# Kernel tuning notes

Measured on AMD Instinct MI355X. Metric: run time of the kernel, lower is better.

## Reference

```python
import jax, jax.numpy as jnp
import numpy as np

H = W = 256
WS = 8          # window size
SHIFT = 4       # shift size
HEADS = 8
DIM = 128
HD = DIM // HEADS
EPS = 1e-5


def _rel_index():
    # Swin-style relative position index, static constant (N=WS*WS)
    coords = np.stack(np.meshgrid(np.arange(WS), np.arange(WS), indexing='ij')).reshape(2, -1)
    rel = coords[:, :, None] - coords[:, None, :]        # (2, N, N)
    rel = rel + (WS - 1)
    return rel[0] * (2 * WS - 1) + rel[1]                # (N, N) in [0, (2WS-1)^2)

_REL_IDX = _rel_index()


def _ln(x, w, b):
    m = jnp.mean(x, axis=-1, keepdims=True)
    v = jnp.var(x, axis=-1, keepdims=True)
    return (x - m) * jax.lax.rsqrt(v + EPS) * w + b


def setup_inputs() -> dict:
    key = jax.random.key(0)
    ks = jax.random.split(key, 8)
    s = 0.02
    return {
        'x': jax.random.normal(ks[0], (2, H * W, DIM), jnp.float32),
        'norm1_w': jnp.ones((DIM,), jnp.float32),
        'norm1_b': jnp.zeros((DIM,), jnp.float32),
        'qkv_w': jax.random.normal(ks[1], (3 * DIM, DIM), jnp.float32) * s,
        'qkv_b': jnp.zeros((3 * DIM,), jnp.float32),
        'rel_bias_table': jax.random.normal(ks[2], ((2 * WS - 1) ** 2, HEADS), jnp.float32) * s,
        'proj_w': jax.random.normal(ks[3], (DIM, DIM), jnp.float32) * s,
        'proj_b': jnp.zeros((DIM,), jnp.float32),
        'norm2_w': jnp.ones((DIM,), jnp.float32),
        'norm2_b': jnp.zeros((DIM,), jnp.float32),
        'fc1_w': jax.random.normal(ks[4], (4 * DIM, DIM), jnp.float32) * s,
        'fc1_b': jnp.zeros((4 * DIM,), jnp.float32),
        'fc2_w': jax.random.normal(ks[5], (DIM, 4 * DIM), jnp.float32) * s,
        'fc2_b': jnp.zeros((DIM,), jnp.float32),
    }


def reference(x, norm1_w, norm1_b, qkv_w, qkv_b, rel_bias_table, proj_w, proj_b,
              norm2_w, norm2_b, fc1_w, fc1_b, fc2_w, fc2_b):
    B, L, C = x.shape
    N = WS * WS
    shortcut = x

    # norm1 -> spatial -> shift (roll only; original applies no attention mask)
    xs = _ln(x, norm1_w, norm1_b).reshape(B, H, W, C)
    xs = jnp.roll(xs, shift=(-SHIFT, -SHIFT), axis=(1, 2))

    # window partition: (B*nH*nW, N, C)
    win = xs.reshape(B, H // WS, WS, W // WS, WS, C)
    win = win.transpose(0, 1, 3, 2, 4, 5).reshape(-1, N, C)

    # window attention
    qkv = (win @ qkv_w.T + qkv_b).reshape(-1, N, 3, HEADS, HD)
    qkv = qkv.transpose(2, 0, 3, 1, 4)                   # (3, nWin, heads, N, hd)
    q, k, v = qkv[0], qkv[1], qkv[2]
    scale = HD ** -0.5
    attn = jnp.einsum('whnd,whmd->whnm', q * scale, k)   # (nWin, heads, N, N)
    bias = rel_bias_table[_REL_IDX]                      # (N, N, heads)
    attn = attn + bias.transpose(2, 0, 1)[None]
    attn = jax.nn.softmax(attn, axis=-1)
    out = jnp.einsum('whnm,whmd->whnd', attn, v)         # (nWin, heads, N, hd)
    out = out.transpose(0, 2, 1, 3).reshape(-1, N, C)
    out = out @ proj_w.T + proj_b

    # window reverse + un-shift
    out = out.reshape(B, H // WS, W // WS, WS, WS, C)
    out = out.transpose(0, 1, 3, 2, 4, 5).reshape(B, H, W, C)
    out = jnp.roll(out, shift=(SHIFT, SHIFT), axis=(1, 2)).reshape(B, L, C)

    x = shortcut + out

    # MLP (fc1 -> exact GELU -> fc2) with residual
    h = _ln(x, norm2_w, norm2_b)
    h = jax.nn.gelu(h @ fc1_w.T + fc1_b, approximate=False)
    h = h @ fc2_w.T + fc2_b
    return x + h
```

## Files before the change

kernel.cpp:

```cpp
#include <hip/hip_runtime.h>
#include <hip/hip_bf16.h>
#include <cmath>

#define LNEPS 1e-5f

typedef __attribute__((ext_vector_type(8))) short short8v;
typedef __attribute__((ext_vector_type(4))) float f32x4;

__device__ __forceinline__ unsigned short f2bf(float f){
  unsigned u = __float_as_uint(f);
  u += 0x7fffu + ((u >> 16) & 1u);
  return (unsigned short)(u >> 16);
}
__device__ __forceinline__ float gelu_f(float x){
  return 0.5f * x * (1.f + erff(x * 0.70710678118654752f));
}
template <int P>
__device__ __forceinline__ void setprio(){
#ifdef __HIP_DEVICE_COMPILE__
  __builtin_amdgcn_s_setprio(P);
#endif
}

__device__ __forceinline__ f32x4 mfma32(short8v a, short8v b, f32x4 c){
#ifdef __HIP_DEVICE_COMPILE__
  return __builtin_amdgcn_mfma_f32_16x16x32_bf16(a, b, c, 0, 0, 0);
#else
  return c;
#endif
}

__device__ __forceinline__ void stage128(const unsigned short* g, int ldg, short* lds){
#ifdef __HIP_DEVICE_COMPILE__
  const int t = threadIdx.x;
  const int wv = t >> 6;
  #pragma unroll
  for (int it = 0; it < 8; ++it) {
    const int flat = it * 256 + t;
    const int r = flat >> 4, c = flat & 15;
    const unsigned short* src = g + (size_t)r * ldg + ((c ^ (r & 7)) << 3);
    short* dst = lds + (size_t)(it * 256 + wv * 64) * 8;
    __builtin_amdgcn_global_load_lds(
        (const __attribute__((address_space(1))) void*)src,
        (__attribute__((address_space(3))) void*)dst, 16, 0, 0);
  }
#else
  (void)g; (void)ldg; (void)lds;
#endif
}
__device__ __forceinline__ void stage128_512(const unsigned short* g, int ldg, short* lds){
#ifdef __HIP_DEVICE_COMPILE__
  const int t = threadIdx.x;
  const int wv = t >> 6;
  #pragma unroll
  for (int it = 0; it < 4; ++it) {
    const int flat = it * 512 + t;
    const int r = flat >> 4, c = flat & 15;
    const unsigned short* src = g + (size_t)r * ldg + ((c ^ (r & 7)) << 3);
    short* dst = lds + (size_t)(it * 512 + wv * 64) * 8;
    __builtin_amdgcn_global_load_lds(
        (const __attribute__((address_space(1))) void*)src,
        (__attribute__((address_space(3))) void*)dst, 16, 0, 0);
  }
#else
  (void)g; (void)ldg; (void)lds;
#endif
}
__device__ __forceinline__ void stage64(const unsigned short* g, short* lds){
#ifdef __HIP_DEVICE_COMPILE__
  const int t = threadIdx.x;
  const int wv = t >> 6;
  #pragma unroll
  for (int it = 0; it < 4; ++it) {
    const int flat = it * 256 + t;
    const int r = flat >> 4, c = flat & 15;
    const unsigned short* src = g + (size_t)r * 128 + ((c ^ (r & 7)) << 3);
    short* dst = lds + (size_t)(it * 256 + wv * 64) * 8;
    __builtin_amdgcn_global_load_lds(
        (const __attribute__((address_space(1))) void*)src,
        (__attribute__((address_space(3))) void*)dst, 16, 0, 0);
  }
#else
  (void)g; (void)lds;
#endif
}
__device__ __forceinline__ short8v frag_ld(const short* lds, int row, int chunk){
  return *(const short8v*)((const char*)lds + row * 256 + ((chunk ^ (row & 7)) << 4));
}

__global__ __launch_bounds__(256) void k0_cvt(
    const float* __restrict__ qkvw, const float* __restrict__ pw,
    const float* __restrict__ w1, const float* __restrict__ w2,
    unsigned short* __restrict__ dst)
{
  const int i = (blockIdx.x * 256 + threadIdx.x) * 4;
  const float* src; int off;
  if (i < 49152)       { src = qkvw; off = i; }
  else if (i < 65536)  { src = pw;   off = i - 49152; }
  else if (i < 131072) { src = w1;   off = i - 65536; }
  else                 { src = w2;   off = i - 131072; }
  const float4 v = *(const float4*)(src + off);
  ushort4 o = { f2bf(v.x), f2bf(v.y), f2bf(v.z), f2bf(v.w) };
  *(ushort4*)(dst + i) = o;
}

__global__ __launch_bounds__(512, 2) void k23_qkv_attn(
    const float* __restrict__ x,
    const float* __restrict__ gw, const float* __restrict__ gb,
    const unsigned short* __restrict__ Wb,
    const float* __restrict__ bias,
    const float* __restrict__ table,
    unsigned short* __restrict__ attn)
{
  __shared__ __align__(16) short At[128 * 128];
  __shared__ __align__(16) short Bt[128 * 128];
  __shared__ __align__(16) short QKl[128 * 256];
  __shared__ float Tb[1800];
  const int t = threadIdx.x;
  const int row0 = blockIdx.x * 128;
  stage128_512(Wb, 128, At);
  for (int i = t; i < 1800; i += 512) Tb[i] = table[i];
  #pragma unroll
  for (int it = 0; it < 4; ++it) {
    const int flat = it * 512 + t;
    const int r = flat >> 4, c = flat & 15;
    const int row = row0 + r;
    const int wid = row >> 6, n = row & 63;
    const int b = wid >> 10, rem = wid & 1023;
    const int wh = rem >> 5, wwi = rem & 31;
    const int i2 = n >> 3, j2 = n & 7;
    const int sh = (wh * 8 + i2 + 4) & 255;
    const int sw = (wwi * 8 + j2 + 4) & 255;
    const float* src = x + (((size_t)b << 16) + sh * 256 + sw) * 128 + c * 8;
    const float4 a0 = *(const float4*)src;
    const float4 a1 = *(const float4*)(src + 4);
    float s  = a0.x + a0.y + a0.z + a0.w + a1.x + a1.y + a1.z + a1.w;
    float ss = a0.x*a0.x + a0.y*a0.y + a0.z*a0.z + a0.w*a0.w
             + a1.x*a1.x + a1.y*a1.y + a1.z*a1.z + a1.w*a1.w;
    s += __shfl_xor(s, 1); ss += __shfl_xor(ss, 1);
    s += __shfl_xor(s, 2); ss += __shfl_xor(ss, 2);
    s += __shfl_xor(s, 4); ss += __shfl_xor(ss, 4);
    s += __shfl_xor(s, 8); ss += __shfl_xor(ss, 8);
    const float mean = s * 0.0078125f;
    const float rstd = rsqrtf(ss * 0.0078125f - mean * mean + LNEPS);
    const float4 g0 = *(const float4*)(gw + c * 8), g1 = *(const float4*)(gw + c * 8 + 4);
    const float4 c0 = *(const float4*)(gb + c * 8), c1 = *(const float4*)(gb + c * 8 + 4);
    uint4 pk;
    pk.x = (unsigned)f2bf((a0.x - mean) * rstd * g0.x + c0.x)
         | ((unsigned)f2bf((a0.y - mean) * rstd * g0.y + c0.y) << 16);
    pk.y = (unsigned)f2bf((a0.z - mean) * rstd * g0.z + c0.z)
         | ((unsigned)f2bf((a0.w - mean) * rstd * g0.w + c0.w) << 16);
    pk.z = (unsigned)f2bf((a1.x - mean) * rstd * g1.x + c1.x)
         | ((unsigned)f2bf((a1.y - mean) * rstd * g1.y + c1.y) << 16);
    pk.w = (unsigned)f2bf((a1.z - mean) * rstd * g1.z + c1.z)
         | ((unsigned)f2bf((a1.w - mean) * rstd * g1.w + c1.w) << 16);
    *(uint4*)((char*)Bt + r * 256 + ((c ^ (r & 7)) << 4)) = pk;
  }
  __syncthreads();

  const int l = t & 63, w = t >> 6, w0 = w & 1, w1 = w >> 1;
  const int g = l >> 4, rl = l & 15;
  const f32x4 z = {0.f, 0.f, 0.f, 0.f};

  for (int nt = 0; nt < 3; ++nt) {
    f32x4 acc[4][2];
    #pragma unroll
    for (int i = 0; i < 4; ++i) { acc[i][0] = z; acc[i][1] = z; }
    #pragma unroll
    for (int kk = 0; kk < 4; ++kk) {
      short8v a[4], b[2];
      #pragma unroll
      for (int i = 0; i < 4; ++i) a[i] = frag_ld(At, w0 * 64 + i * 16 + rl, kk * 4 + g);
      #pragma unroll
      for (int j = 0; j < 2; ++j) b[j] = frag_ld(Bt, w1 * 32 + j * 16 + rl, kk * 4 + g);
      #pragma unroll
      for (int i = 0; i < 4; ++i)
        #pragma unroll
        for (int j = 0; j < 2; ++j)
          acc[i][j] = mfma32(a[i], b[j], acc[i][j]);
    }
    if (nt < 2) {
      #pragma unroll
      for (int i = 0; i < 4; ++i) {
        const int c = w0 * 64 + i * 16 + 4 * g;
        const float4 bv = *(const float4*)(bias + nt * 128 + c);
        const int chunk = nt * 16 + (c >> 3), inner = (c & 7) * 2;
        #pragma unroll
        for (int j = 0; j < 2; ++j) {
          const int r = w1 * 32 + j * 16 + rl;
          ushort4 o = { f2bf(acc[i][j][0] + bv.x), f2bf(acc[i][j][1] + bv.y),
                        f2bf(acc[i][j][2] + bv.z), f2bf(acc[i][j][3] + bv.w) };
          *(ushort4*)((char*)QKl + r * 512 + ((chunk ^ (r & 7)) << 4) + inner) = o;
        }
      }
      __syncthreads();
      stage128_512(Wb + (size_t)(nt + 1) * 16384, 128, At);
      __syncthreads();
    } else {
      __syncthreads();
      #pragma unroll
      for (int i = 0; i < 4; ++i) {
        const int c = w0 * 64 + i * 16 + 4 * g;
        const int h2 = c >> 4, db = c & 15;
        const float4 bv = *(const float4*)(bias + 256 + c);
        const float ba[4] = {bv.x, bv.y, bv.z, bv.w};
        #pragma unroll
        for (int j = 0; j < 2; ++j) {
          const int r = w1 * 32 + j * 16 + rl;
          const int wl = r >> 6, m = r & 63;
          char* vb = (char*)Bt + (wl * 8 + h2) * 2048;
          #pragma unroll
          for (int e = 0; e < 4; ++e) {
            const int d = db + e;
            *(unsigned short*)(vb + d * 128 + (((m >> 3) ^ (d & 7)) << 4) + (m & 7) * 2)
                = f2bf(acc[i][j][e] + ba[e]);
          }
        }
      }
      __syncthreads();
    }
  }

  const int h = w;
  char* Pw = (char*)At + w * 4096;
  const short8v zz = {0,0,0,0,0,0,0,0};
  for (int wl = 0; wl < 2; ++wl) {
    const int win = blockIdx.x * 2 + wl;
    short8v qf[4], kf[4];
    if (g < 2) {
      #pragma unroll
      for (int rf = 0; rf < 4; ++rf) {
        const int r = wl * 64 + rf * 16 + rl;
        qf[rf] = *(const short8v*)((char*)QKl + r * 512 + (((2 * h + g) ^ (r & 7)) << 4));
      }
      #pragma unroll
      for (int mf = 0; mf < 4; ++mf) {
        const int r = wl * 64 + mf * 16 + rl;
        kf[mf] = *(const short8v*)((char*)QKl + r * 512 + (((16 + 2 * h + g) ^ (r & 7)) << 4));
      }
    } else {
      #pragma unroll
      for (int i = 0; i < 4; ++i) { qf[i] = zz; kf[i] = zz; }
    }
    f32x4 s[4][4];
    #pragma unroll
    for (int mf = 0; mf < 4; ++mf)
      #pragma unroll
      for (int rf = 0; rf < 4; ++rf)
        s[mf][rf] = mfma32(kf[mf], qf[rf], z);
    float sum[4];
    #pragma unroll
    for (int rf = 0; rf < 4; ++rf) {
      const int r = rf * 16 + rl, i1 = r >> 3, j1 = r & 7;
      float mx = -1e30f;
      #pragma unroll
      for (int mf = 0; mf < 4; ++mf)
        #pragma unroll
        for (int e = 0; e < 4; ++e) {
          const int m = mf * 16 + g * 4 + e;
          const int i2 = m >> 3, j2 = m & 7;
          const float v = s[mf][rf][e] * 0.25f + Tb[((i1 - i2 + 7) * 15 + (j1 - j2 + 7)) * 8 + h];
          s[mf][rf][e] = v;
          mx = fmaxf(mx, v);
        }
      mx = fmaxf(mx, __shfl_xor(mx, 16));
      mx = fmaxf(mx, __shfl_xor(mx, 32));
      float sm = 0.f;
      #pragma unroll
      for (int mf = 0; mf < 4; ++mf)
        #pragma unroll
        for (int e = 0; e < 4; ++e) {
          const float ev = __expf(s[mf][rf][e] - mx);
          s[mf][rf][e] = ev;
          sm += ev;
        }
      sm += __shfl_xor(sm, 16);
      sm += __shfl_xor(sm, 32);
      sum[rf] = sm;
    }
    const char* vbase = (char*)Bt + (wl * 8 + h) * 2048;
    f32x4 o[4];
    #pragma unroll
    for (int rf = 0; rf < 4; ++rf) o[rf] = z;
    #pragma unroll
    for (int hm = 0; hm < 2; ++hm) {
      #pragma unroll
      for (int rf = 0; rf < 4; ++rf) {
        const int r = rf * 16 + rl;
        #pragma unroll
        for (int mfl = 0; mfl < 2; ++mfl) {
          const int mf = hm * 2 + mfl;
          uint2 u;
          u.x = (unsigned)f2bf(s[mf][rf][0]) | ((unsigned)f2bf(s[mf][rf][1]) << 16);
          u.y = (unsigned)f2bf(s[mf][rf][2]) | ((unsigned)f2bf(s[mf][rf][3]) << 16);
          *(uint2*)(Pw + r * 64 + (((mfl * 2 + (g >> 1)) ^ ((r >> 1) & 3)) << 4) + (g & 1) * 8) = u;
        }
      }
      const short8v va = *(const short8v*)(vbase + rl * 128 + (((hm * 4 + g) ^ (rl & 7)) << 4));
      #pragma unroll
      for (int rf = 0; rf < 4; ++rf) {
        const int r = rf * 16 + rl;
        const short8v pb = *(const short8v*)(Pw + r * 64 + ((g ^ ((r >> 1) & 3)) << 4));
        o[rf] = mfma32(va, pb, o[rf]);
      }
    }
    #pragma unroll
    for (int rf = 0; rf < 4; ++rf) {
      const float inv = 1.f / sum[rf];
      const int r = rf * 16 + rl;
      ushort4 ov = { f2bf(o[rf][0] * inv), f2bf(o[rf][1] * inv),
                     f2bf(o[rf][2] * inv), f2bf(o[rf][3] * inv) };
      *(ushort4*)(attn + ((size_t)win * 64 + r) * 128 + h * 16 + g * 4) = ov;
    }
  }
}

__global__ __launch_bounds__(256, 2) void k45_proj_mlp(
    const unsigned short* __restrict__ A,
    const unsigned short* __restrict__ pwb,
    const float* __restrict__ pb,
    const float* __restrict__ xin,
    const float* __restrict__ gw, const float* __restrict__ gb,
    const unsigned short* __restrict__ w1b, const float* __restrict__ b1,
    const unsigned short* __restrict__ w2b, const float* __restrict__ b2,
    float* __restrict__ out)
{
  __shared__ __align__(16) short Xt[64 * 128];
  __shared__ __align__(16) short Ht[64 * 128];
  __shared__ __align__(16) short Wt[128 * 128];
  __shared__ float2 Gt[1024];
  __shared__ float2 Red[64 * 8];
  const int t = threadIdx.x;
  const int row0 = blockIdx.x * 64;
  stage128(pwb, 128, Wt);
  stage64(A + (size_t)row0 * 128, Ht);
  #pragma unroll
  for (int i = t; i < 1024; i += 256) {
    const float x0 = (float)i * 0.0078125f - 4.f;
    const float g0 = gelu_f(x0);
    Gt[i] = make_float2(g0, gelu_f(x0 + 0.0078125f) - g0);
  }
  const int l = t & 63, w = t >> 6, w0 = w & 1, w1 = w >> 1;
  const int g = l >> 4, rl = l & 15;
  size_t obase[2];
  float4 xv[4][2];
  #pragma unroll
  for (int j = 0; j < 2; ++j) {
    const int r = row0 + w1 * 32 + j * 16 + rl;
    const int wn = r >> 6, n = r & 63;
    const int b_ = wn >> 10, rem = wn & 1023;
    const int wh = rem >> 5, ww = rem & 31;
    const int si = n >> 3, sj = n & 7;
    const int hd = (wh * 8 + si + 4) & 255;
    const int wd = (ww * 8 + sj + 4) & 255;
    obase[j] = (((size_t)b_ << 16) + hd * 256 + wd) * 128;
    #pragma unroll
    for (int i = 0; i < 4; ++i)
      xv[i][j] = *(const float4*)(xin + obase[j] + w0 * 64 + i * 16 + 4 * g);
  }
  __syncthreads();
  const f32x4 z = {0.f, 0.f, 0.f, 0.f};
  f32x4 x2r[4][2];
  #pragma unroll
  for (int i = 0; i < 4; ++i) { x2r[i][0] = z; x2r[i][1] = z; }
  setprio<1>();
  #pragma unroll
  for (int kk = 0; kk < 4; ++kk) {
    short8v a[4], b[2];
    #pragma unroll
    for (int i = 0; i < 4; ++i) a[i] = frag_ld(Wt, w0 * 64 + i * 16 + rl, kk * 4 + g);
    #pragma unroll
    for (int j = 0; j < 2; ++j) b[j] = frag_ld(Ht, w1 * 32 + j * 16 + rl, kk * 4 + g);
    #pragma unroll
    for (int i = 0; i < 4; ++i)
      #pragma unroll
      for (int j = 0; j < 2; ++j)
        x2r[i][j] = mfma32(a[i], b[j], x2r[i][j]);
  }
  setprio<0>();
  #pragma unroll
  for (int i = 0; i < 4; ++i) {
    const float4 bv = *(const float4*)(pb + w0 * 64 + i * 16 + 4 * g);
    #pragma unroll
    for (int j = 0; j < 2; ++j) {
      x2r[i][j][0] += xv[i][j].x + bv.x;
      x2r[i][j][1] += xv[i][j].y + bv.y;
      x2r[i][j][2] += xv[i][j].z + bv.z;
      x2r[i][j][3] += xv[i][j].w + bv.w;
    }
  }
  #pragma unroll
  for (int j = 0; j < 2; ++j) {
    float s = 0.f, ss = 0.f;
    #pragma unroll
    for (int i = 0; i < 4; ++i)
      #pragma unroll
      for (int e = 0; e < 4; ++e) { const float v = x2r[i][j][e]; s += v; ss += v * v; }
    Red[(w1 * 32 + j * 16 + rl) * 8 + (w0 * 4 + g)] = make_float2(s, ss);
  }
  __syncthreads();
  float mean[2], rstd[2];
  #pragma unroll
  for (int j = 0; j < 2; ++j) {
    const float2* rp = &Red[(w1 * 32 + j * 16 + rl) * 8];
    float s = 0.f, ss = 0.f;
    #pragma unroll
    for (int k = 0; k < 8; ++k) { s += rp[k].x; ss += rp[k].y; }
    mean[j] = s * 0.0078125f;
    rstd[j] = rsqrtf(ss * 0.0078125f - mean[j] * mean[j] + LNEPS);
  }
  #pragma unroll
  for (int i = 0; i < 4; ++i) {
    const int c = w0 * 64 + i * 16 + 4 * g;
    const float4 g4 = *(const float4*)(gw + c);
    const float4 c4 = *(const float4*)(gb + c);
    #pragma unroll
    for (int j = 0; j < 2; ++j) {
      const int r = w1 * 32 + j * 16 + rl;
      ushort4 p;
      p.x = f2bf((x2r[i][j][0] - mean[j]) * rstd[j] * g4.x + c4.x);
      p.y = f2bf((x2r[i][j][1] - mean[j]) * rstd[j] * g4.y + c4.y);
      p.z = f2bf((x2r[i][j][2] - mean[j]) * rstd[j] * g4.z + c4.z);
      p.w = f2bf((x2r[i][j][3] - mean[j]) * rstd[j] * g4.w + c4.w);
      const int chunk = c >> 3, inner = (c & 7) * 2;
      *(ushort4*)((char*)Xt + r * 256 + ((chunk ^ (r & 7)) << 4) + inner) = p;
    }
  }
  f32x4 oacc[4][2];
  #pragma unroll
  for (int i = 0; i < 4; ++i) { oacc[i][0] = z; oacc[i][1] = z; }
  for (int sb = 0; sb < 4; ++sb) {
    __syncthreads();
    stage128(w1b + (size_t)sb * 128 * 128, 128, Wt);
    __syncthreads();
    f32x4 hacc[4][2];
    #pragma unroll
    for (int i = 0; i < 4; ++i) { hacc[i][0] = z; hacc[i][1] = z; }
    setprio<1>();
    #pragma unroll
    for (int kk = 0; kk < 4; ++kk) {
      short8v a[4], b[2];
      #pragma unroll
      for (int i = 0; i < 4; ++i) a[i] = frag_ld(Wt, w0 * 64 + i * 16 + rl, kk * 4 + g);
      #pragma unroll
      for (int j = 0; j < 2; ++j) b[j] = frag_ld(Xt, w1 * 32 + j * 16 + rl, kk * 4 + g);
      #pragma unroll
      for (int i = 0; i < 4; ++i)
        #pragma unroll
        for (int j = 0; j < 2; ++j)
          hacc[i][j] = mfma32(a[i], b[j], hacc[i][j]);
    }
    setprio<0>();
    __syncthreads();
    stage128(w2b + (size_t)sb * 128, 512, Wt);
    #pragma unroll
    for (int i = 0; i < 4; ++i) {
      const int cl = w0 * 64 + i * 16 + 4 * g;
      const float4 b1v = *(const float4*)(b1 + sb * 128 + cl);
      const float ba[4] = {b1v.x, b1v.y, b1v.z, b1v.w};
      #pragma unroll
      for (int j = 0; j < 2; ++j) {
        const int r = w1 * 32 + j * 16 + rl;
        unsigned short pe[4];
        #pragma unroll
        for (int e = 0; e < 4; ++e) {
          const float xh = hacc[i][j][e] + ba[e];
          float tq = fmaf(xh, 128.f, 512.f);
          tq = fminf(fmaxf(tq, 0.f), 1023.99f);
          const float fi = floorf(tq);
          const float2 ent = Gt[(int)fi];
          float gv = fmaf(tq - fi, ent.y, ent.x);
          gv = xh > 3.98f ? xh : gv;
          pe[e] = f2bf(gv);
        }
        ushort4 p = { pe[0], pe[1], pe[2], pe[3] };
        const int chunk = cl >> 3, inner = (cl & 7) * 2;
        *(ushort4*)((char*)Ht + r * 256 + ((chunk ^ (r & 7)) << 4) + inner) = p;
      }
    }
    __syncthreads();
    setprio<1>();
    #pragma unroll
    for (int kk = 0; kk < 4; ++kk) {
      short8v a[4], b[2];
      #pragma unroll
      for (int i = 0; i < 4; ++i) a[i] = frag_ld(Wt, w0 * 64 + i * 16 + rl, kk * 4 + g);
      #pragma unroll
      for (int j = 0; j < 2; ++j) b[j] = frag_ld(Ht, w1 * 32 + j * 16 + rl, kk * 4 + g);
      #pragma unroll
      for (int i = 0; i < 4; ++i)
        #pragma unroll
        for (int j = 0; j < 2; ++j)
          oacc[i][j] = mfma32(a[i], b[j], oacc[i][j]);
    }
    setprio<0>();
  }
  #pragma unroll
  for (int i = 0; i < 4; ++i) {
    const int c = w0 * 64 + i * 16 + 4 * g;
    const float4 bv = *(const float4*)(b2 + c);
    #pragma unroll
    for (int j = 0; j < 2; ++j) {
      float4 o = { x2r[i][j][0] + oacc[i][j][0] + bv.x,
                   x2r[i][j][1] + oacc[i][j][1] + bv.y,
                   x2r[i][j][2] + oacc[i][j][2] + bv.z,
                   x2r[i][j][3] + oacc[i][j][3] + bv.w };
      *(float4*)(out + obase[j] + c) = o;
    }
  }
}

extern "C" void kernel_launch(void* const* d_in, const int* in_sizes, int n_in,
                              void* d_out, int out_size, void* d_ws, size_t ws_size,
                              hipStream_t stream)
{
  const float* x    = (const float*)d_in[0];
  const float* n1w  = (const float*)d_in[1];
  const float* n1b  = (const float*)d_in[2];
  const float* qkvw = (const float*)d_in[3];
  const float* qkvB = (const float*)d_in[4];
  const float* relb = (const float*)d_in[5];
  const float* pw   = (const float*)d_in[6];
  const float* pb   = (const float*)d_in[7];
  const float* n2w  = (const float*)d_in[8];
  const float* n2b  = (const float*)d_in[9];
  const float* w1   = (const float*)d_in[10];
  const float* b1   = (const float*)d_in[11];
  const float* w2   = (const float*)d_in[12];
  const float* b2   = (const float*)d_in[13];
  float* out = (float*)d_out;

  unsigned short* winb = (unsigned short*)d_ws;
  unsigned short* wb   = winb + 16777216;
  unsigned short* qkvw_b = wb;
  unsigned short* pw_b   = wb + 49152;
  unsigned short* w1_b   = wb + 65536;
  unsigned short* w2_b   = wb + 131072;

  k0_cvt<<<192, 256, 0, stream>>>(qkvw, pw, w1, w2, wb);
  k23_qkv_attn<<<1024, 512, 0, stream>>>(x, n1w, n1b, qkvw_b, qkvB, relb, winb);
  k45_proj_mlp<<<2048, 256, 0, stream>>>(winb, pw_b, pb, x, n2w, n2b,
                                         w1_b, b1, w2_b, b2, out);
}
```

Baseline: 175.3 us.

## Process one window per block and precompute expanded relative-position bias

The QKV+attention kernel now handles one 64-token window per 256-thread block instead of two windows per 512-thread block, with each wave covering two heads of that window. LDS use per block drops by removing the second window's Q/K/V buffers and the staged bias table. A new small kernel expands the relative-position bias table into a dense (heads, N, N) float array in workspace, and the softmax reads it with float4 global loads instead of doing index arithmetic and LDS gathers. The cost is that the QKV weight tile is staged twice as often across the grid, plus an extra launch and bias traffic from global/L2.

```diff
diff --git a/kernel.cpp b/kernel.cpp
--- a/kernel.cpp
+++ b/kernel.cpp
@@ -40,24 +40,6 @@
     const int r = flat >> 4, c = flat & 15;
     const unsigned short* src = g + (size_t)r * ldg + ((c ^ (r & 7)) << 3);
     short* dst = lds + (size_t)(it * 256 + wv * 64) * 8;
-    __builtin_amdgcn_global_load_lds(
-        (const __attribute__((address_space(1))) void*)src,
-        (__attribute__((address_space(3))) void*)dst, 16, 0, 0);
-  }
-#else
-  (void)g; (void)ldg; (void)lds;
-#endif
-}
-__device__ __forceinline__ void stage128_512(const unsigned short* g, int ldg, short* lds){
-#ifdef __HIP_DEVICE_COMPILE__
-  const int t = threadIdx.x;
-  const int wv = t >> 6;
-  #pragma unroll
-  for (int it = 0; it < 4; ++it) {
-    const int flat = it * 512 + t;
-    const int r = flat >> 4, c = flat & 15;
-    const unsigned short* src = g + (size_t)r * ldg + ((c ^ (r & 7)) << 3);
-    short* dst = lds + (size_t)(it * 512 + wv * 64) * 8;
     __builtin_amdgcn_global_load_lds(
         (const __attribute__((address_space(1))) void*)src,
         (__attribute__((address_space(3))) void*)dst, 16, 0, 0);
@@ -104,25 +86,43 @@
   *(ushort4*)(dst + i) = o;
 }
 
-__global__ __launch_bounds__(512, 2) void k23_qkv_attn(
+__global__ __launch_bounds__(256) void k0b_bias(
+    const float* __restrict__ table, float* __restrict__ be)
+{
+  const int i = blockIdx.x * 256 + threadIdx.x;
+  const int m4 = (i & 15) * 4;
+  const int r  = (i >> 4) & 63;
+  const int h  = i >> 10;
+  const int i1 = r >> 3, j1 = r & 7;
+  float o[4];
+  #pragma unroll
+  for (int e = 0; e < 4; ++e) {
+    const int m = m4 + e;
+    const int i2 = m >> 3, j2 = m & 7;
+    o[e] = table[((i1 - i2 + 7) * 15 + (j1 - j2 + 7)) * 8 + h];
+  }
+  float4 ov = { o[0], o[1], o[2], o[3] };
+  *(float4*)(be + ((h * 64 + r) * 64 + m4)) = ov;
+}
+
+__global__ __launch_bounds__(256, 2) void k23_qkv_attn(
     const float* __restrict__ x,
     const float* __restrict__ gw, const float* __restrict__ gb,
     const unsigned short* __restrict__ Wb,
     const float* __restrict__ bias,
-    const float* __restrict__ table,
+    const float* __restrict__ be,
     unsigned short* __restrict__ attn)
 {
   __shared__ __align__(16) short At[128 * 128];
-  __shared__ __align__(16) short Bt[128 * 128];
-  __shared__ __align__(16) short QKl[128 * 256];
-  __shared__ float Tb[1800];
+  __shared__ __align__(16) short Bt[64 * 128];
+  __shared__ __align__(16) short QK[64 * 256];
   const int t = threadIdx.x;
-  const int row0 = blockIdx.x * 128;
-  stage128_512(Wb, 128, At);
-  for (int i = t; i < 1800; i += 512) Tb[i] = table[i];
+  const int win = blockIdx.x;
+  const int row0 = win * 64;
+  stage128(Wb, 128, At);
   #pragma unroll
   for (int it = 0; it < 4; ++it) {
-    const int flat = it * 512 + t;
+    const int flat = it * 256 + t;
     const int r = flat >> 4, c = flat & 15;
     const int row = row0 + r;
     const int wid = row >> 6, n = row & 63;
@@ -190,11 +190,11 @@
           const int r = w1 * 32 + j * 16 + rl;
           ushort4 o = { f2bf(acc[i][j][0] + bv.x), f2bf(acc[i][j][1] + bv.y),
                         f2bf(acc[i][j][2] + bv.z), f2bf(acc[i][j][3] + bv.w) };
-          *(ushort4*)((char*)QKl + r * 512 + ((chunk ^ (r & 7)) << 4) + inner) = o;
+          *(ushort4*)((char*)QK + r * 512 + ((chunk ^ (r & 7)) << 4) + inner) = o;
         }
       }
       __syncthreads();
-      stage128_512(Wb + (size_t)(nt + 1) * 16384, 128, At);
+      stage128(Wb + (size_t)(nt + 1) * 16384, 128, At);
       __syncthreads();
     } else {
       __syncthreads();
@@ -206,9 +206,8 @@
         const float ba[4] = {bv.x, bv.y, bv.z, bv.w};
         #pragma unroll
         for (int j = 0; j < 2; ++j) {
-          const int r = w1 * 32 + j * 16 + rl;
-          const int wl = r >> 6, m = r & 63;
-          char* vb = (char*)Bt + (wl * 8 + h2) * 2048;
+          const int m = w1 * 32 + j * 16 + rl;
+          char* vb = (char*)Bt + h2 * 2048;
           #pragma unroll
           for (int e = 0; e < 4; ++e) {
             const int d = db + e;
@@ -221,22 +220,21 @@
     }
   }
 
-  const int h = w;
   char* Pw = (char*)At + w * 4096;
   const short8v zz = {0,0,0,0,0,0,0,0};
-  for (int wl = 0; wl < 2; ++wl) {
-    const int win = blockIdx.x * 2 + wl;
+  for (int hh = 0; hh < 2; ++hh) {
+    const int h = w * 2 + hh;
     short8v qf[4], kf[4];
     if (g < 2) {
       #pragma unroll
       for (int rf = 0; rf < 4; ++rf) {
-        const int r = wl * 64 + rf * 16 + rl;
-        qf[rf] = *(const short8v*)((char*)QKl + r * 512 + (((2 * h + g) ^ (r & 7)) << 4));
+        const int r = rf * 16 + rl;
+        qf[rf] = *(const short8v*)((char*)QK + r * 512 + (((2 * h + g) ^ (r & 7)) << 4));
       }
       #pragma unroll
       for (int mf = 0; mf < 4; ++mf) {
-        const int r = wl * 64 + mf * 16 + rl;
-        kf[mf] = *(const short8v*)((char*)QKl + r * 512 + (((16 + 2 * h + g) ^ (r & 7)) << 4));
+        const int r = mf * 16 + rl;
+        kf[mf] = *(const short8v*)((char*)QK + r * 512 + (((16 + 2 * h + g) ^ (r & 7)) << 4));
       }
     } else {
       #pragma unroll
@@ -251,18 +249,20 @@
     float sum[4];
     #pragma unroll
     for (int rf = 0; rf < 4; ++rf) {
-      const int r = rf * 16 + rl, i1 = r >> 3, j1 = r & 7;
+      const int r = rf * 16 + rl;
+      const float* bp = be + (size_t)(h * 64 + r) * 64;
       float mx = -1e30f;
       #pragma unroll
-      for (int mf = 0; mf < 4; ++mf)
+      for (int mf = 0; mf < 4; ++mf) {
+        const float4 bv = *(const float4*)(bp + mf * 16 + g * 4);
+        const float ba[4] = {bv.x, bv.y, bv.z, bv.w};
         #pragma unroll
         for (int e = 0; e < 4; ++e) {
-          const int m = mf * 16 + g * 4 + e;
-          const int i2 = m >> 3, j2 = m & 7;
-          const float v = s[mf][rf][e] * 0.25f + Tb[((i1 - i2 + 7) * 15 + (j1 - j2 + 7)) * 8 + h];
+          const float v = s[mf][rf][e] * 0.25f + ba[e];
           s[mf][rf][e] = v;
           mx = fmaxf(mx, v);
         }
+      }
       mx = fmaxf(mx, __shfl_xor(mx, 16));
       mx = fmaxf(mx, __shfl_xor(mx, 32));
       float sm = 0.f;
@@ -278,7 +278,7 @@
       sm += __shfl_xor(sm, 32);
       sum[rf] = sm;
     }
-    const char* vbase = (char*)Bt + (wl * 8 + h) * 2048;
+    const char* vbase = (char*)Bt + h * 2048;
     f32x4 o[4];
     #pragma unroll
     for (int rf = 0; rf < 4; ++rf) o[rf] = z;
@@ -536,9 +536,11 @@
   unsigned short* pw_b   = wb + 49152;
   unsigned short* w1_b   = wb + 65536;
   unsigned short* w2_b   = wb + 131072;
+  float* be = (float*)(wb + 196608);
 
   k0_cvt<<<192, 256, 0, stream>>>(qkvw, pw, w1, w2, wb);
-  k23_qkv_attn<<<1024, 512, 0, stream>>>(x, n1w, n1b, qkvw_b, qkvB, relb, winb);
+  k0b_bias<<<32, 256, 0, stream>>>(relb, be);
+  k23_qkv_attn<<<2048, 256, 0, stream>>>(x, n1w, n1b, qkvw_b, qkvB, be, winb);
   k45_proj_mlp<<<2048, 256, 0, stream>>>(winb, pw_b, pb, x, n2w, n2b,
                                          w1_b, b1, w2_b, b2, out);
 }
```

After: 171.9 us. Within noise of the previous version (-1.9%).
